# Kernel optimization log

Measured on AMD Instinct MI355X. Metric: run time of the kernel, lower is better.

The kernel has to match this reference:

```python
import jax, jax.numpy as jnp
import numpy as np

B, S, D, H = 4, 2048, 1024, 16
HD = D // H  # head size = 64


def setup_inputs() -> dict:
    key = jax.random.key(0)
    ks = jax.random.split(key, 9)
    scale = 1.0 / np.sqrt(D)
    x = jax.random.normal(ks[0], (B, S, D), dtype=jnp.float32)
    Wq = jax.random.normal(ks[1], (D, D), dtype=jnp.float32) * scale
    Wk = jax.random.normal(ks[2], (D, D), dtype=jnp.float32) * scale
    Wv = jax.random.normal(ks[3], (D, D), dtype=jnp.float32) * scale
    Wo = jax.random.normal(ks[4], (D, D), dtype=jnp.float32) * scale
    bq = jax.random.normal(ks[5], (D,), dtype=jnp.float32) * 0.01
    bk = jax.random.normal(ks[6], (D,), dtype=jnp.float32) * 0.01
    bv = jax.random.normal(ks[7], (D,), dtype=jnp.float32) * 0.01
    bo = jax.random.normal(ks[8], (D,), dtype=jnp.float32) * 0.01
    return {"x": x, "Wq": Wq, "bq": bq, "Wk": Wk, "bk": bk,
            "Wv": Wv, "bv": bv, "Wo": Wo, "bo": bo}


def reference(x, Wq, bq, Wk, bk, Wv, bv, Wo, bo):
    Bv, Sv, Dv = x.shape
    # QKV projections (torch Linear: x @ W^T + b; here W stored as [in, out])
    q = x @ Wq + bq  # [B,S,D]
    k = x @ Wk + bk
    v = x @ Wv + bv
    # split heads -> [B,H,S,HD]
    q = q.reshape(Bv, Sv, H, HD).transpose(0, 2, 1, 3)
    k = k.reshape(Bv, Sv, H, HD).transpose(0, 2, 1, 3)
    v = v.reshape(Bv, Sv, H, HD).transpose(0, 2, 1, 3)
    # scaled scores + additive causal mask (upper triangle -> -inf)
    scores = jnp.einsum('bhqd,bhkd->bhqk', q, k) * (1.0 / np.sqrt(HD))
    causal = jnp.triu(jnp.full((Sv, Sv), -jnp.inf, dtype=scores.dtype), k=1)
    attn = jax.nn.softmax(scores + causal, axis=-1)
    # dropout is identity in eval / p=0
    out = jnp.einsum('bhqk,bhkd->bhqd', attn, v)
    out = out.transpose(0, 2, 1, 3).reshape(Bv, Sv, Dv)
    return out @ Wo + bo
```

## Files before the change

kernel.cpp:

```cpp
#include <hip/hip_runtime.h>
#include <hip/hip_bf16.h>


typedef unsigned short u16;
typedef short bf16x8 __attribute__((ext_vector_type(8)));
typedef float f32x4 __attribute__((ext_vector_type(4)));

constexpr int NB = 4, NS = 2048, ND = 1024, NH = 16, NHD = 64;
constexpr int NM = NB * NS;
constexpr float NEG = -1e30f;
constexpr int EPAD = 136;
constexpr float KEXP = 0.125f * 1.4426950408889634f;

#if __has_builtin(__builtin_amdgcn_exp2f)
#define EXP2(x) __builtin_amdgcn_exp2f(x)
#else
#define EXP2(x) exp2f(x)
#endif

__device__ __forceinline__ u16 f2bf(float f) {
  union { float f; unsigned int u; } c; c.f = f;
  unsigned int r = (c.u + 0x7FFFu + ((c.u >> 16) & 1u)) >> 16;
  return (u16)r;
}
__device__ __forceinline__ unsigned int pk2bf(float a, float b) {
  float2 t; t.x = a; t.y = b;
  __hip_bfloat162 h = __float22bfloat162_rn(t);
  unsigned int u; __builtin_memcpy(&u, &h, 4); return u;
}
__device__ __forceinline__ void g2lds16(const u16* g, u16* l) {
  __builtin_amdgcn_global_load_lds(
      (const __attribute__((address_space(1))) void*)g,
      (__attribute__((address_space(3))) void*)l, 16, 0, 0);
}
__device__ __forceinline__ bf16x8 ldsw(const u16* b, int row, int cq) {
  return *(const bf16x8*)&b[row * 64 + ((cq ^ (row & 7)) << 3)];
}

__global__ __launch_bounds__(256) void fill_kernel(float* __restrict__ p, float v, int n) {
  int i = blockIdx.x * 256 + threadIdx.x;
  if (i < n) p[i] = v;
}

__global__ __launch_bounds__(256) void cvt_kernel(const float* __restrict__ in,
                                                  u16* __restrict__ out, int n4) {
  int i = blockIdx.x * 256 + threadIdx.x;
  if (i < n4) {
    float4 f = ((const float4*)in)[i];
    ushort4 o;
    o.x = f2bf(f.x); o.y = f2bf(f.y); o.z = f2bf(f.z); o.w = f2bf(f.w);
    ((ushort4*)out)[i] = o;
  }
}

__global__ __launch_bounds__(256) void wt_kernel(
    const float* __restrict__ s0, const float* __restrict__ s1,
    const float* __restrict__ s2, const float* __restrict__ s3,
    u16* __restrict__ d0, u16* __restrict__ d1,
    u16* __restrict__ d2, u16* __restrict__ d3) {
  const int z = blockIdx.z;
  const float* S = (z == 0) ? s0 : (z == 1) ? s1 : (z == 2) ? s2 : s3;
  u16* D = (z == 0) ? d0 : (z == 1) ? d1 : (z == 2) ? d2 : d3;
  const float sc = (z == 0) ? KEXP : 1.0f;
  __shared__ u16 t[64][68];
  const int r0 = blockIdx.x * 64, c0 = blockIdx.y * 64;
  const int tid = threadIdx.x;
#pragma unroll
  for (int i = 0; i < 4; i++) {
    int row = (tid >> 4) + i * 16;
    int col = (tid & 15) * 4;
    float4 f = *(const float4*)&S[(long)(r0 + row) * ND + c0 + col];
    ushort4 u;
    u.x = f2bf(f.x * sc); u.y = f2bf(f.y * sc);
    u.z = f2bf(f.z * sc); u.w = f2bf(f.w * sc);
    *(ushort4*)&t[row][col] = u;
  }
  __syncthreads();
#pragma unroll
  for (int i = 0; i < 4; i++) {
    int nrow = (tid >> 4) + i * 16;
    int kcol = (tid & 15) * 4;
    ushort4 u;
    u.x = t[kcol + 0][nrow]; u.y = t[kcol + 1][nrow];
    u.z = t[kcol + 2][nrow]; u.w = t[kcol + 3][nrow];
    *(ushort4*)&D[(long)(c0 + nrow) * ND + r0 + kcol] = u;
  }
}

__global__ __launch_bounds__(256, 3) void gemm_qkv_kernel(
    const float* __restrict__ Xf, const u16* __restrict__ Xb,
    const u16* __restrict__ WtQ,
    const float* __restrict__ bqp, const float* __restrict__ bkp,
    const float* __restrict__ bvp,
    u16* __restrict__ Qw, u16* __restrict__ Kw, u16* __restrict__ Vtw,
    int xmode) {
  __shared__ __attribute__((aligned(16))) u16 SMEM[128 * EPAD];
  u16* Asm = SMEM;
  u16* Bsm = SMEM + 8192;
  const int m0 = blockIdx.x * 128;
  const int ng = blockIdx.y;
  const int mat = ng >> 3, n0 = (ng & 7) * 128;
  const u16* Wt = WtQ + (long)mat * ND * ND;
  const int tid = threadIdx.x;
  const int w = tid >> 6, lane = tid & 63, quad = lane >> 4, lr = lane & 15;
  const int wm = w & 1, wn = w >> 1;
  const int b_r = lane >> 3, b_c = lane & 7;

  f32x4 acc[4][4] = {};

  for (int k0 = 0; k0 < ND; k0 += 64) {
    __syncthreads();
    if (xmode == 0) {
#pragma unroll
      for (int j = 0; j < 4; j++) {
        int r = w * 32 + j * 8 + b_r;
        const float* src = Xf + (long)(m0 + r) * ND + k0 + ((b_c ^ (r & 7)) << 3);
        float4 f0 = *(const float4*)src;
        float4 f1 = *(const float4*)(src + 4);
        uint4 d;
        d.x = pk2bf(f0.x, f0.y); d.y = pk2bf(f0.z, f0.w);
        d.z = pk2bf(f1.x, f1.y); d.w = pk2bf(f1.z, f1.w);
        *(uint4*)&Asm[r * 64 + (b_c << 3)] = d;
      }
    } else {
#pragma unroll
      for (int j = 0; j < 4; j++) {
        int R0 = w * 32 + j * 8;
        int r = R0 + b_r;
        g2lds16(Xb + (long)(m0 + r) * ND + k0 + ((b_c ^ (r & 7)) << 3),
                &Asm[R0 * 64]);
      }
    }
#pragma unroll
    for (int j = 0; j < 4; j++) {
      int R0 = w * 32 + j * 8;
      int r = R0 + b_r;
      g2lds16(Wt + (long)(n0 + r) * ND + k0 + ((b_c ^ (r & 7)) << 3),
              &Bsm[R0 * 64]);
    }
    __syncthreads();

#pragma unroll
    for (int kk = 0; kk < 2; kk++) {
      bf16x8 af[4], bfr[4];
#pragma unroll
      for (int mt = 0; mt < 4; mt++)
        af[mt] = ldsw(Asm, wm * 64 + mt * 16 + lr, kk * 4 + quad);
#pragma unroll
      for (int nt = 0; nt < 4; nt++)
        bfr[nt] = ldsw(Bsm, wn * 64 + nt * 16 + lr, kk * 4 + quad);
#pragma unroll
      for (int nt = 0; nt < 4; nt++)
#pragma unroll
        for (int mt = 0; mt < 4; mt++)
          acc[nt][mt] = __builtin_amdgcn_mfma_f32_16x16x32_bf16(
              af[mt], bfr[nt], acc[nt][mt], 0, 0, 0);
    }
  }

  const float* bias = (mat == 0) ? bqp : (mat == 1) ? bkp : bvp;
  const float bsc = (mat == 0) ? KEXP : 1.0f;
  __syncthreads();
  if (mat < 2) {
#pragma unroll
    for (int nt = 0; nt < 4; nt++) {
      int n_loc = wn * 64 + nt * 16 + lr;
      float bn = bias[n0 + n_loc] * bsc;
#pragma unroll
      for (int mt = 0; mt < 4; mt++)
#pragma unroll
        for (int r = 0; r < 4; r++) {
          int m_loc = wm * 64 + mt * 16 + quad * 4 + r;
          SMEM[m_loc * EPAD + n_loc] = f2bf(acc[nt][mt][r] + bn);
        }
    }
    __syncthreads();
    u16* Yv = (mat == 0) ? Qw : Kw;
#pragma unroll
    for (int pass = 0; pass < 8; pass++) {
      int row = pass * 16 + (tid >> 4), c = tid & 15;
      uint4 d = *(const uint4*)&SMEM[row * EPAD + c * 8];
      int n_g = n0 + c * 8, h_ = n_g >> 6, hd_ = n_g & (NHD - 1);
      int m = m0 + row, b_ = m >> 11, s_ = m & (NS - 1);
      *(uint4*)&Yv[((long)((b_ * NH + h_) * NS + s_)) * NHD + hd_] = d;
    }
  } else {
#pragma unroll
    for (int nt = 0; nt < 4; nt++) {
      int n_loc = wn * 64 + nt * 16 + lr;
      float bn = bias[n0 + n_loc];
#pragma unroll
      for (int mt = 0; mt < 4; mt++) {
        int m_base = wm * 64 + mt * 16 + quad * 4;
        uint2 d;
        d.x = pk2bf(acc[nt][mt][0] + bn, acc[nt][mt][1] + bn);
        d.y = pk2bf(acc[nt][mt][2] + bn, acc[nt][mt][3] + bn);
        *(uint2*)&SMEM[n_loc * EPAD + m_base] = d;
      }
    }
    __syncthreads();
#pragma unroll
    for (int pass = 0; pass < 8; pass++) {
      int plane = pass * 16 + (tid >> 4), mc = tid & 15;
      uint4 d = *(const uint4*)&SMEM[plane * EPAD + mc * 8];
      int n_g = n0 + plane, h_ = n_g >> 6, hd_ = n_g & (NHD - 1);
      int m = m0 + mc * 8, b_ = m >> 11, s_ = m & (NS - 1);
      long base = ((long)((b_ * NH + h_) * NHD + hd_)) * NS;
      int cb = s_ & ~31;
      int s1 = (mc & 1) * 16 + ((mc >> 1) & 1) * 4;
      uint2 lo; lo.x = d.x; lo.y = d.y;
      uint2 hi; hi.x = d.z; hi.y = d.w;
      *(uint2*)&Vtw[base + cb + s1] = lo;
      *(uint2*)&Vtw[base + cb + s1 + 8] = hi;
    }
  }
}

__global__ __launch_bounds__(256, 3) void gemm_out_kernel(
    const u16* __restrict__ Xg, const u16* __restrict__ Wt,
    const float* __restrict__ bias, float* __restrict__ Y) {
  __shared__ __attribute__((aligned(16))) u16 Asm[128 * 64];
  __shared__ __attribute__((aligned(16))) u16 Bsm[128 * 64];
  const int m0 = blockIdx.x * 128, n0 = blockIdx.y * 128;
  const int tid = threadIdx.x;
  const int w = tid >> 6, lane = tid & 63, quad = lane >> 4, lr = lane & 15;
  const int wm = w & 1, wn = w >> 1;
  const int b_r = lane >> 3, b_c = lane & 7;

  f32x4 acc[4][4] = {};

  for (int k0 = 0; k0 < ND; k0 += 64) {
    __syncthreads();
    const int h_ = k0 >> 6;
#pragma unroll
    for (int j = 0; j < 4; j++) {
      int R0 = w * 32 + j * 8;
      int r = R0 + b_r;
      int mrow = m0 + r, b_ = mrow >> 11, s_ = mrow & (NS - 1);
      g2lds16(Xg + ((long)((b_ * NH + h_) * NS + s_)) * NHD + ((b_c ^ (r & 7)) << 3),
              &Asm[R0 * 64]);
      g2lds16(Wt + (long)(n0 + r) * ND + k0 + ((b_c ^ (r & 7)) << 3),
              &Bsm[R0 * 64]);
    }
    __syncthreads();

#pragma unroll
    for (int kk = 0; kk < 2; kk++) {
      bf16x8 af[4], bfr[4];
#pragma unroll
      for (int mt = 0; mt < 4; mt++)
        af[mt] = ldsw(Asm, wm * 64 + mt * 16 + lr, kk * 4 + quad);
#pragma unroll
      for (int nt = 0; nt < 4; nt++)
        bfr[nt] = ldsw(Bsm, wn * 64 + nt * 16 + lr, kk * 4 + quad);
#pragma unroll
      for (int nt = 0; nt < 4; nt++)
#pragma unroll
        for (int mt = 0; mt < 4; mt++)
          acc[nt][mt] = __builtin_amdgcn_mfma_f32_16x16x32_bf16(
              af[mt], bfr[nt], acc[nt][mt], 0, 0, 0);
    }
  }

#pragma unroll
  for (int nt = 0; nt < 4; nt++) {
    int n = n0 + wn * 64 + nt * 16 + lr;
    float bn = bias[n];
#pragma unroll
    for (int mt = 0; mt < 4; mt++) {
#pragma unroll
      for (int r = 0; r < 4; r++) {
        int m = m0 + wm * 64 + mt * 16 + quad * 4 + r;
        Y[(long)m * ND + n] = acc[nt][mt][r] + bn;
      }
    }
  }
}

__global__ __launch_bounds__(512) void attn_kernel(
    u16* __restrict__ Q, const u16* __restrict__ K, const u16* __restrict__ Vtg) {
  __shared__ __attribute__((aligned(16))) u16 Klds[64 * 64];
  __shared__ __attribute__((aligned(16))) u16 Vt[64 * 64];
  const int bh = blockIdx.x;
  const int qt = 15 - blockIdx.y;
  const int q0 = qt * 128;
  const int tid = threadIdx.x;
  const int w = tid >> 6, lane = tid & 63, quad = lane >> 4, lr = lane & 15;
  u16* Qb = Q + (long)bh * NS * NHD;
  const u16* Kb = K + (long)bh * NS * NHD;
  const u16* Vb = Vtg + (long)bh * NHD * NS;

  const int qw0 = q0 + w * 16;
  bf16x8 qf[2];
  {
    int m = qw0 + lr;
    qf[0] = *(const bf16x8*)&Qb[(long)m * NHD + quad * 8];
    qf[1] = *(const bf16x8*)&Qb[(long)m * NHD + 32 + quad * 8];
  }
  const bf16x8 ones = {0x3F80, 0x3F80, 0x3F80, 0x3F80,
                       0x3F80, 0x3F80, 0x3F80, 0x3F80};

  f32x4 oaccT[4] = {};
  f32x4 lacc = {};

  const int sr = lane >> 3;
  const int ssw = (((lane & 7) ^ sr) << 3);
  const int krow0 = w * 8;
  const int jmax = q0 + 64;

  for (int j0 = 0; j0 <= jmax; j0 += 64) {
    __syncthreads();
    g2lds16(Kb + (long)(j0 + krow0 + sr) * NHD + ssw, &Klds[krow0 * 64]);
    g2lds16(Vb + (long)(krow0 + sr) * NS + j0 + ssw, &Vt[krow0 * 64]);
    __syncthreads();

    if (j0 > qw0 + 15) continue;

    f32x4 scT[4] = {};
#pragma unroll
    for (int t = 0; t < 4; t++) {
      int kr = t * 16 + lr;
      bf16x8 kf0 = ldsw(Klds, kr, quad);
      bf16x8 kf1 = ldsw(Klds, kr, 4 + quad);
      scT[t] = __builtin_amdgcn_mfma_f32_16x16x32_bf16(kf0, qf[0], scT[t], 0, 0, 0);
      scT[t] = __builtin_amdgcn_mfma_f32_16x16x32_bf16(kf1, qf[1], scT[t], 0, 0, 0);
    }

    if (j0 + 63 > qw0) {
#pragma unroll
      for (int t = 0; t < 4; t++)
#pragma unroll
        for (int r = 0; r < 4; r++)
          if ((j0 + t * 16 + quad * 4 + r) > (qw0 + lr)) scT[t][r] = NEG;
    }

#pragma unroll
    for (int t = 0; t < 4; t++)
#pragma unroll
      for (int r = 0; r < 4; r++) scT[t][r] = EXP2(scT[t][r]);

#pragma unroll
    for (int kk = 0; kk < 2; kk++) {
      uint4 pu;
      pu.x = pk2bf(scT[2 * kk][0], scT[2 * kk][1]);
      pu.y = pk2bf(scT[2 * kk][2], scT[2 * kk][3]);
      pu.z = pk2bf(scT[2 * kk + 1][0], scT[2 * kk + 1][1]);
      pu.w = pk2bf(scT[2 * kk + 1][2], scT[2 * kk + 1][3]);
      bf16x8 pt; __builtin_memcpy(&pt, &pu, 16);
      lacc = __builtin_amdgcn_mfma_f32_16x16x32_bf16(ones, pt, lacc, 0, 0, 0);
#pragma unroll
      for (int dt = 0; dt < 4; dt++) {
        bf16x8 va = ldsw(Vt, dt * 16 + lr, kk * 4 + quad);
        oaccT[dt] = __builtin_amdgcn_mfma_f32_16x16x32_bf16(va, pt, oaccT[dt], 0, 0, 0);
      }
    }
  }

  const float inv = 1.0f / lacc[0];
#pragma unroll
  for (int dt = 0; dt < 4; dt++) {
    uint2 o;
    o.x = pk2bf(oaccT[dt][0] * inv, oaccT[dt][1] * inv);
    o.y = pk2bf(oaccT[dt][2] * inv, oaccT[dt][3] * inv);
    *(uint2*)&Qb[(long)(qw0 + lr) * NHD + dt * 16 + quad * 4] = o;
  }
}

extern "C" void kernel_launch(void* const* d_in, const int* in_sizes, int n_in,
                              void* d_out, int out_size, void* d_ws, size_t ws_size,
                              hipStream_t stream) {
  const float* x  = (const float*)d_in[0];
  const float* Wq = (const float*)d_in[1];
  const float* bq = (const float*)d_in[2];
  const float* Wk = (const float*)d_in[3];
  const float* bk = (const float*)d_in[4];
  const float* Wv = (const float*)d_in[5];
  const float* bv = (const float*)d_in[6];
  const float* Wo = (const float*)d_in[7];
  const float* bo = (const float*)d_in[8];

  const size_t BUF = (size_t)NM * ND * sizeof(u16);
  if (ws_size < 2 * BUF) {
    fill_kernel<<<(out_size + 255) / 256, 256, 0, stream>>>((float*)d_out, 0.f, out_size);
    return;
  }

  u16* Qw  = (u16*)d_ws;
  u16* Vtw = Qw + (long)NM * ND;
  u16* Kw  = (u16*)d_out;
  u16* WtQ = Kw + (long)NM * ND;
  u16* WtO = WtQ + 3L * ND * ND;
  const bool bigws = ws_size >= 3 * BUF;
  u16* Xb = bigws ? (Vtw + (long)NM * ND) : nullptr;

  wt_kernel<<<dim3(16, 16, 4), 256, 0, stream>>>(Wq, Wk, Wv, Wo,
      WtQ, WtQ + (long)ND * ND, WtQ + 2L * ND * ND, WtO);
  if (bigws)
    cvt_kernel<<<(NM * ND / 4 + 255) / 256, 256, 0, stream>>>(x, Xb, NM * ND / 4);

  gemm_qkv_kernel<<<dim3(64, 24), 256, 0, stream>>>(
      x, Xb, WtQ, bq, bk, bv, Qw, Kw, Vtw, bigws ? 2 : 0);
  attn_kernel<<<dim3(NB * NH, NS / 128), 512, 0, stream>>>(Qw, Kw, Vtw);
  hipMemcpyAsync(Vtw, WtO, (size_t)ND * ND * sizeof(u16),
                 hipMemcpyDeviceToDevice, stream);
  gemm_out_kernel<<<dim3(64, 8), 256, 0, stream>>>(Qw, Vtw, bo, (float*)d_out);
}
```

Baseline: 230.4 us.

## Add 256x128-tile double-buffered QKV GEMM with 8 waves and grid swizzle

Adds a new QKV projection kernel that runs when the bf16 copy of x is available. It uses 512 threads and a 256x128 output tile per block, with double-buffered LDS staging via direct global-to-LDS loads, explicit vmcnt/lgkmcnt waits and barriers, and s_setprio around the MFMA bursts. It also swizzles the block index for L2 locality. The aim is to overlap memory loads with matrix math and raise arithmetic intensity per block, at the cost of one block per CU and a heavier LDS footprint. The old kernel is kept as the fp32-input fallback.

After: 241.2 us. 4.7% more time.

```diff
diff --git a/kernel.cpp b/kernel.cpp
--- a/kernel.cpp
+++ b/kernel.cpp
@@ -87,13 +87,178 @@
   }
 }
 
-__global__ __launch_bounds__(256, 3) void gemm_qkv_kernel(
-    const float* __restrict__ Xf, const u16* __restrict__ Xb,
-    const u16* __restrict__ WtQ,
+__global__ __launch_bounds__(512, 1) void gemm_qkv8_kernel(
+    const u16* __restrict__ Xb, const u16* __restrict__ WtQ,
     const float* __restrict__ bqp, const float* __restrict__ bkp,
     const float* __restrict__ bvp,
-    u16* __restrict__ Qw, u16* __restrict__ Kw, u16* __restrict__ Vtw,
-    int xmode) {
+    u16* __restrict__ Qw, u16* __restrict__ Kw, u16* __restrict__ Vtw) {
+  __shared__ __attribute__((aligned(16))) u16 SM[49152];
+  const int bid = blockIdx.x;
+  const int swz = (bid & 7) * 96 + (bid >> 3);
+  const int tm = swz / 24, tn = swz % 24;
+  const int m0 = tm * 256;
+  const int mat = tn >> 3, n0 = (tn & 7) * 128;
+  const u16* Wt = WtQ + (long)mat * ND * ND;
+  const int tid = threadIdx.x;
+  const int w = tid >> 6, lane = tid & 63, quad = lane >> 4, lr = lane & 15;
+  const int wm = w >> 2, wn = w & 3;
+  const int srow = tid >> 3, sc = tid & 7;
+  const int scol = (sc ^ (srow & 7)) << 3;
+
+  f32x4 acc[8][2] = {};
+
+#define STAGE_AQ(d, q, t)                                                  \
+  g2lds16(Xb + (long)(m0 + (q) * 64 + srow) * ND + (t) * 64 + scol,        \
+          &SM[(d) * 16384 + (q) * 4096 + w * 512])
+#define STAGE_BH(d, j, t)                                                  \
+  g2lds16(Wt + (long)(n0 + (j) * 64 + srow) * ND + (t) * 64 + scol,        \
+          &SM[32768 + (d) * 8192 + (j) * 4096 + w * 512])
+
+#pragma unroll
+  for (int t = 0; t < 2; t++) {
+    STAGE_AQ(t, 0, t); STAGE_AQ(t, 2, t);
+    STAGE_BH(t, 0, t); STAGE_BH(t, 1, t);
+    STAGE_AQ(t, 1, t); STAGE_AQ(t, 3, t);
+  }
+  asm volatile("s_waitcnt vmcnt(6)" ::: "memory");
+  __builtin_amdgcn_s_barrier();
+  __builtin_amdgcn_sched_barrier(0);
+
+  bf16x8 bfr[2][2];
+#pragma unroll 2
+  for (int t = 0; t < 16; ++t) {
+    const int d = t & 1;
+    const u16* Ad = &SM[d * 16384];
+    const u16* Bd = &SM[32768 + d * 8192];
+    bf16x8 af[4][2];
+#pragma unroll
+    for (int mf = 0; mf < 4; mf++) {
+      int ar = wm * 128 + mf * 16 + lr;
+#pragma unroll
+      for (int kk = 0; kk < 2; kk++)
+        af[mf][kk] = ldsw(&Ad[(ar >> 6) * 4096], ar & 63, kk * 4 + quad);
+    }
+#pragma unroll
+    for (int nf = 0; nf < 2; nf++) {
+      int br = wn * 32 + nf * 16 + lr;
+#pragma unroll
+      for (int kk = 0; kk < 2; kk++)
+        bfr[nf][kk] = ldsw(Bd, br, kk * 4 + quad);
+    }
+    if (t >= 1 && t + 1 < 16) {
+      STAGE_AQ(d ^ 1, 1, t + 1); STAGE_AQ(d ^ 1, 3, t + 1);
+    }
+    __builtin_amdgcn_s_barrier();
+    asm volatile("s_waitcnt lgkmcnt(0)" ::: "memory");
+    __builtin_amdgcn_sched_barrier(0);
+    __builtin_amdgcn_s_setprio(1);
+#pragma unroll
+    for (int mf = 0; mf < 4; mf++)
+#pragma unroll
+      for (int nf = 0; nf < 2; nf++)
+#pragma unroll
+        for (int kk = 0; kk < 2; kk++)
+          acc[mf][nf] = __builtin_amdgcn_mfma_f32_16x16x32_bf16(
+              af[mf][kk], bfr[nf][kk], acc[mf][nf], 0, 0, 0);
+    __builtin_amdgcn_s_setprio(0);
+    if (t == 15) asm volatile("s_waitcnt vmcnt(0)" ::: "memory");
+    else         asm volatile("s_waitcnt vmcnt(6)" ::: "memory");
+    __builtin_amdgcn_s_barrier();
+    __builtin_amdgcn_sched_barrier(0);
+    bf16x8 ag[4][2];
+#pragma unroll
+    for (int mf = 0; mf < 4; mf++) {
+      int ar = wm * 128 + (mf + 4) * 16 + lr;
+#pragma unroll
+      for (int kk = 0; kk < 2; kk++)
+        ag[mf][kk] = ldsw(&Ad[(ar >> 6) * 4096], ar & 63, kk * 4 + quad);
+    }
+    if (t + 2 < 16) {
+      STAGE_AQ(d, 0, t + 2); STAGE_AQ(d, 2, t + 2);
+      STAGE_BH(d, 0, t + 2); STAGE_BH(d, 1, t + 2);
+    }
+    __builtin_amdgcn_s_barrier();
+    asm volatile("s_waitcnt lgkmcnt(0)" ::: "memory");
+    __builtin_amdgcn_sched_barrier(0);
+    __builtin_amdgcn_s_setprio(1);
+#pragma unroll
+    for (int mf = 0; mf < 4; mf++)
+#pragma unroll
+      for (int nf = 0; nf < 2; nf++)
+#pragma unroll
+        for (int kk = 0; kk < 2; kk++)
+          acc[4 + mf][nf] = __builtin_amdgcn_mfma_f32_16x16x32_bf16(
+              ag[mf][kk], bfr[nf][kk], acc[4 + mf][nf], 0, 0, 0);
+    __builtin_amdgcn_s_setprio(0);
+    asm volatile("s_waitcnt vmcnt(6)" ::: "memory");
+    __builtin_amdgcn_s_barrier();
+    __builtin_amdgcn_sched_barrier(0);
+  }
+#undef STAGE_AQ
+#undef STAGE_BH
+
+  const float* bias = (mat == 0) ? bqp : (mat == 1) ? bkp : bvp;
+  const float bsc = (mat == 0) ? KEXP : 1.0f;
+  if (mat < 2) {
+#pragma unroll
+    for (int nf = 0; nf < 2; nf++) {
+      int n_loc = wn * 32 + nf * 16 + lr;
+      float bn = bias[n0 + n_loc] * bsc;
+#pragma unroll
+      for (int mf = 0; mf < 8; mf++)
+#pragma unroll
+        for (int r = 0; r < 4; r++) {
+          int m_loc = wm * 128 + mf * 16 + quad * 4 + r;
+          SM[m_loc * EPAD + n_loc] = f2bf(acc[mf][nf][r] + bn);
+        }
+    }
+    __syncthreads();
+    u16* Yv = (mat == 0) ? Qw : Kw;
+#pragma unroll
+    for (int pass = 0; pass < 8; pass++) {
+      int row = pass * 32 + (tid >> 4), c = tid & 15;
+      uint4 dta = *(const uint4*)&SM[row * EPAD + c * 8];
+      int n_g = n0 + c * 8, h_ = n_g >> 6, hd_ = n_g & (NHD - 1);
+      int m = m0 + row, b_ = m >> 11, s_ = m & (NS - 1);
+      *(uint4*)&Yv[((long)((b_ * NH + h_) * NS + s_)) * NHD + hd_] = dta;
+    }
+  } else {
+#pragma unroll
+    for (int nf = 0; nf < 2; nf++) {
+      int n_loc = wn * 32 + nf * 16 + lr;
+      float bn = bias[n0 + n_loc];
+#pragma unroll
+      for (int mf = 0; mf < 8; mf++) {
+        int m_base = wm * 128 + mf * 16 + quad * 4;
+        uint2 dta;
+        dta.x = pk2bf(acc[mf][nf][0] + bn, acc[mf][nf][1] + bn);
+        dta.y = pk2bf(acc[mf][nf][2] + bn, acc[mf][nf][3] + bn);
+        *(uint2*)&SM[n_loc * 264 + m_base] = dta;
+      }
+    }
+    __syncthreads();
+#pragma unroll
+    for (int pass = 0; pass < 8; pass++) {
+      int plane = pass * 16 + (tid >> 5), mc = tid & 31;
+      uint4 dta = *(const uint4*)&SM[plane * 264 + mc * 8];
+      int n_g = n0 + plane, h_ = n_g >> 6, hd_ = n_g & (NHD - 1);
+      int m = m0 + mc * 8, b_ = m >> 11, s_ = m & (NS - 1);
+      long base = ((long)((b_ * NH + h_) * NHD + hd_)) * NS;
+      int cb = s_ & ~31;
+      int s1 = (mc & 1) * 16 + ((mc >> 1) & 1) * 4;
+      uint2 lo; lo.x = dta.x; lo.y = dta.y;
+      uint2 hi; hi.x = dta.z; hi.y = dta.w;
+      *(uint2*)&Vtw[base + cb + s1] = lo;
+      *(uint2*)&Vtw[base + cb + s1 + 8] = hi;
+    }
+  }
+}
+
+__global__ __launch_bounds__(256, 3) void gemm_qkv_kernel(
+    const float* __restrict__ Xf, const u16* __restrict__ WtQ,
+    const float* __restrict__ bqp, const float* __restrict__ bkp,
+    const float* __restrict__ bvp,
+    u16* __restrict__ Qw, u16* __restrict__ Kw, u16* __restrict__ Vtw) {
   __shared__ __attribute__((aligned(16))) u16 SMEM[128 * EPAD];
   u16* Asm = SMEM;
   u16* Bsm = SMEM + 8192;
@@ -110,26 +275,16 @@
 
   for (int k0 = 0; k0 < ND; k0 += 64) {
     __syncthreads();
-    if (xmode == 0) {
-#pragma unroll
-      for (int j = 0; j < 4; j++) {
-        int r = w * 32 + j * 8 + b_r;
-        const float* src = Xf + (long)(m0 + r) * ND + k0 + ((b_c ^ (r & 7)) << 3);
-        float4 f0 = *(const float4*)src;
-        float4 f1 = *(const float4*)(src + 4);
-        uint4 d;
-        d.x = pk2bf(f0.x, f0.y); d.y = pk2bf(f0.z, f0.w);
-        d.z = pk2bf(f1.x, f1.y); d.w = pk2bf(f1.z, f1.w);
-        *(uint4*)&Asm[r * 64 + (b_c << 3)] = d;
-      }
-    } else {
-#pragma unroll
-      for (int j = 0; j < 4; j++) {
-        int R0 = w * 32 + j * 8;
-        int r = R0 + b_r;
-        g2lds16(Xb + (long)(m0 + r) * ND + k0 + ((b_c ^ (r & 7)) << 3),
-                &Asm[R0 * 64]);
-      }
+#pragma unroll
+    for (int j = 0; j < 4; j++) {
+      int r = w * 32 + j * 8 + b_r;
+      const float* src = Xf + (long)(m0 + r) * ND + k0 + ((b_c ^ (r & 7)) << 3);
+      float4 f0 = *(const float4*)src;
+      float4 f1 = *(const float4*)(src + 4);
+      uint4 dta;
+      dta.x = pk2bf(f0.x, f0.y); dta.y = pk2bf(f0.z, f0.w);
+      dta.z = pk2bf(f1.x, f1.y); dta.w = pk2bf(f1.z, f1.w);
+      *(uint4*)&Asm[r * 64 + (b_c << 3)] = dta;
     }
 #pragma unroll
     for (int j = 0; j < 4; j++) {
@@ -179,10 +334,10 @@
 #pragma unroll
     for (int pass = 0; pass < 8; pass++) {
       int row = pass * 16 + (tid >> 4), c = tid & 15;
-      uint4 d = *(const uint4*)&SMEM[row * EPAD + c * 8];
+      uint4 dta = *(const uint4*)&SMEM[row * EPAD + c * 8];
       int n_g = n0 + c * 8, h_ = n_g >> 6, hd_ = n_g & (NHD - 1);
       int m = m0 + row, b_ = m >> 11, s_ = m & (NS - 1);
-      *(uint4*)&Yv[((long)((b_ * NH + h_) * NS + s_)) * NHD + hd_] = d;
+      *(uint4*)&Yv[((long)((b_ * NH + h_) * NS + s_)) * NHD + hd_] = dta;
     }
   } else {
 #pragma unroll
@@ -192,24 +347,24 @@
 #pragma unroll
       for (int mt = 0; mt < 4; mt++) {
         int m_base = wm * 64 + mt * 16 + quad * 4;
-        uint2 d;
-        d.x = pk2bf(acc[nt][mt][0] + bn, acc[nt][mt][1] + bn);
-        d.y = pk2bf(acc[nt][mt][2] + bn, acc[nt][mt][3] + bn);
-        *(uint2*)&SMEM[n_loc * EPAD + m_base] = d;
+        uint2 dta;
+        dta.x = pk2bf(acc[nt][mt][0] + bn, acc[nt][mt][1] + bn);
+        dta.y = pk2bf(acc[nt][mt][2] + bn, acc[nt][mt][3] + bn);
+        *(uint2*)&SMEM[n_loc * EPAD + m_base] = dta;
       }
     }
     __syncthreads();
 #pragma unroll
     for (int pass = 0; pass < 8; pass++) {
       int plane = pass * 16 + (tid >> 4), mc = tid & 15;
-      uint4 d = *(const uint4*)&SMEM[plane * EPAD + mc * 8];
+      uint4 dta = *(const uint4*)&SMEM[plane * EPAD + mc * 8];
       int n_g = n0 + plane, h_ = n_g >> 6, hd_ = n_g & (NHD - 1);
       int m = m0 + mc * 8, b_ = m >> 11, s_ = m & (NS - 1);
       long base = ((long)((b_ * NH + h_) * NHD + hd_)) * NS;
       int cb = s_ & ~31;
       int s1 = (mc & 1) * 16 + ((mc >> 1) & 1) * 4;
-      uint2 lo; lo.x = d.x; lo.y = d.y;
-      uint2 hi; hi.x = d.z; hi.y = d.w;
+      uint2 lo; lo.x = dta.x; lo.y = dta.y;
+      uint2 hi; hi.x = dta.z; hi.y = dta.w;
       *(uint2*)&Vtw[base + cb + s1] = lo;
       *(uint2*)&Vtw[base + cb + s1 + 8] = hi;
     }
@@ -395,11 +550,14 @@
 
   wt_kernel<<<dim3(16, 16, 4), 256, 0, stream>>>(Wq, Wk, Wv, Wo,
       WtQ, WtQ + (long)ND * ND, WtQ + 2L * ND * ND, WtO);
-  if (bigws)
+  if (bigws) {
     cvt_kernel<<<(NM * ND / 4 + 255) / 256, 256, 0, stream>>>(x, Xb, NM * ND / 4);
-
-  gemm_qkv_kernel<<<dim3(64, 24), 256, 0, stream>>>(
-      x, Xb, WtQ, bq, bk, bv, Qw, Kw, Vtw, bigws ? 2 : 0);
+    gemm_qkv8_kernel<<<768, 512, 0, stream>>>(
+        Xb, WtQ, bq, bk, bv, Qw, Kw, Vtw);
+  } else {
+    gemm_qkv_kernel<<<dim3(64, 24), 256, 0, stream>>>(
+        x, WtQ, bq, bk, bv, Qw, Kw, Vtw);
+  }
   attn_kernel<<<dim3(NB * NH, NS / 128), 512, 0, stream>>>(Qw, Kw, Vtw);
   hipMemcpyAsync(Vtw, WtO, (size_t)ND * ND * sizeof(u16),
                  hipMemcpyDeviceToDevice, stream);
```

## Double-buffer K/V tiles in attention kernel with async prefetch

Applied to the files above, without the earlier changes.

The attention loop now keeps two LDS buffers for K and V tiles. It prefetches the next tile with direct global-to-LDS loads while the current tile is processed, and uses an explicit vmcnt wait plus raw barriers instead of two __syncthreads per iteration. The aim is to hide global load latency behind the MFMA and exp work. In exchange it doubles LDS use and depends on the manual vmcnt count matching the number of outstanding loads.

After: 234.7 us. About the same (+1.9%).

```diff
diff --git a/kernel.cpp b/kernel.cpp
--- a/kernel.cpp
+++ b/kernel.cpp
@@ -279,8 +279,8 @@
 
 __global__ __launch_bounds__(512) void attn_kernel(
     u16* __restrict__ Q, const u16* __restrict__ K, const u16* __restrict__ Vtg) {
-  __shared__ __attribute__((aligned(16))) u16 Klds[64 * 64];
-  __shared__ __attribute__((aligned(16))) u16 Vt[64 * 64];
+  __shared__ __attribute__((aligned(16))) u16 Klds[2][64 * 64];
+  __shared__ __attribute__((aligned(16))) u16 Vt[2][64 * 64];
   const int bh = blockIdx.x;
   const int qt = 15 - blockIdx.y;
   const int q0 = qt * 128;
@@ -306,54 +306,66 @@
   const int sr = lane >> 3;
   const int ssw = (((lane & 7) ^ sr) << 3);
   const int krow0 = w * 8;
-  const int jmax = q0 + 64;
-
-  for (int j0 = 0; j0 <= jmax; j0 += 64) {
-    __syncthreads();
-    g2lds16(Kb + (long)(j0 + krow0 + sr) * NHD + ssw, &Klds[krow0 * 64]);
-    g2lds16(Vb + (long)(krow0 + sr) * NS + j0 + ssw, &Vt[krow0 * 64]);
-    __syncthreads();
-
-    if (j0 > qw0 + 15) continue;
-
-    f32x4 scT[4] = {};
-#pragma unroll
-    for (int t = 0; t < 4; t++) {
-      int kr = t * 16 + lr;
-      bf16x8 kf0 = ldsw(Klds, kr, quad);
-      bf16x8 kf1 = ldsw(Klds, kr, 4 + quad);
-      scT[t] = __builtin_amdgcn_mfma_f32_16x16x32_bf16(kf0, qf[0], scT[t], 0, 0, 0);
-      scT[t] = __builtin_amdgcn_mfma_f32_16x16x32_bf16(kf1, qf[1], scT[t], 0, 0, 0);
-    }
-
-    if (j0 + 63 > qw0) {
+  const int ntile = q0 / 64 + 2;
+
+  g2lds16(Kb + (long)(krow0 + sr) * NHD + ssw, &Klds[0][krow0 * 64]);
+  g2lds16(Vb + (long)(krow0 + sr) * NS + 0 + ssw, &Vt[0][krow0 * 64]);
+
+  for (int ti = 0; ti < ntile; ti++) {
+    const int j0 = ti * 64;
+    const int cur = ti & 1;
+    if (ti + 1 < ntile) {
+      const int j1 = j0 + 64;
+      g2lds16(Kb + (long)(j1 + krow0 + sr) * NHD + ssw, &Klds[cur ^ 1][krow0 * 64]);
+      g2lds16(Vb + (long)(krow0 + sr) * NS + j1 + ssw, &Vt[cur ^ 1][krow0 * 64]);
+      asm volatile("s_waitcnt vmcnt(2)" ::: "memory");
+    } else {
+      asm volatile("s_waitcnt vmcnt(0)" ::: "memory");
+    }
+    __builtin_amdgcn_s_barrier();
+    __builtin_amdgcn_sched_barrier(0);
+
+    if (j0 <= qw0 + 15) {
+      f32x4 scT[4] = {};
+#pragma unroll
+      for (int t = 0; t < 4; t++) {
+        int kr = t * 16 + lr;
+        bf16x8 kf0 = ldsw(Klds[cur], kr, quad);
+        bf16x8 kf1 = ldsw(Klds[cur], kr, 4 + quad);
+        scT[t] = __builtin_amdgcn_mfma_f32_16x16x32_bf16(kf0, qf[0], scT[t], 0, 0, 0);
+        scT[t] = __builtin_amdgcn_mfma_f32_16x16x32_bf16(kf1, qf[1], scT[t], 0, 0, 0);
+      }
+
+      if (j0 + 63 > qw0) {
+#pragma unroll
+        for (int t = 0; t < 4; t++)
+#pragma unroll
+          for (int r = 0; r < 4; r++)
+            if ((j0 + t * 16 + quad * 4 + r) > (qw0 + lr)) scT[t][r] = NEG;
+      }
+
 #pragma unroll
       for (int t = 0; t < 4; t++)
 #pragma unroll
-        for (int r = 0; r < 4; r++)
-          if ((j0 + t * 16 + quad * 4 + r) > (qw0 + lr)) scT[t][r] = NEG;
-    }
-
-#pragma unroll
-    for (int t = 0; t < 4; t++)
-#pragma unroll
-      for (int r = 0; r < 4; r++) scT[t][r] = EXP2(scT[t][r]);
-
-#pragma unroll
-    for (int kk = 0; kk < 2; kk++) {
-      uint4 pu;
-      pu.x = pk2bf(scT[2 * kk][0], scT[2 * kk][1]);
-      pu.y = pk2bf(scT[2 * kk][2], scT[2 * kk][3]);
-      pu.z = pk2bf(scT[2 * kk + 1][0], scT[2 * kk + 1][1]);
-      pu.w = pk2bf(scT[2 * kk + 1][2], scT[2 * kk + 1][3]);
-      bf16x8 pt; __builtin_memcpy(&pt, &pu, 16);
-      lacc = __builtin_amdgcn_mfma_f32_16x16x32_bf16(ones, pt, lacc, 0, 0, 0);
-#pragma unroll
-      for (int dt = 0; dt < 4; dt++) {
-        bf16x8 va = ldsw(Vt, dt * 16 + lr, kk * 4 + quad);
-        oaccT[dt] = __builtin_amdgcn_mfma_f32_16x16x32_bf16(va, pt, oaccT[dt], 0, 0, 0);
-      }
-    }
+        for (int r = 0; r < 4; r++) scT[t][r] = EXP2(scT[t][r]);
+
+#pragma unroll
+      for (int kk = 0; kk < 2; kk++) {
+        uint4 pu;
+        pu.x = pk2bf(scT[2 * kk][0], scT[2 * kk][1]);
+        pu.y = pk2bf(scT[2 * kk][2], scT[2 * kk][3]);
+        pu.z = pk2bf(scT[2 * kk + 1][0], scT[2 * kk + 1][1]);
+        pu.w = pk2bf(scT[2 * kk + 1][2], scT[2 * kk + 1][3]);
+        bf16x8 pt; __builtin_memcpy(&pt, &pu, 16);
+        lacc = __builtin_amdgcn_mfma_f32_16x16x32_bf16(ones, pt, lacc, 0, 0, 0);
+#pragma unroll
+        for (int dt = 0; dt < 4; dt++) {
+          bf16x8 va = ldsw(Vt[cur], dt * 16 + lr, kk * 4 + quad);
+          oaccT[dt] = __builtin_amdgcn_mfma_f32_16x16x32_bf16(va, pt, oaccT[dt], 0, 0, 0);
+        }
+      }
+    }
+    __builtin_amdgcn_s_barrier();
   }
 
   const float inv = 1.0f / lacc[0];
```
